# Kernel tuning notes

Hardware: AMD Instinct MI355X
Metric: run time of the kernel (lower is better)

Reference implementation:

```python
import jax, jax.numpy as jnp
import numpy as np

B, T = 16, 512
LAT, ACT, TSK = 512, 64, 96
E, NH, HD = 1024, 16, 64
L, HID, MAXS = 4, 4096, 512


def setup_inputs() -> dict:
    key = jax.random.key(0)
    ks = jax.random.split(key, 16)
    def rn(k, shape, std=0.02):
        return jax.random.normal(k, shape, jnp.float32) * std
    return {
        "z": jax.random.normal(ks[0], (B, T, LAT), jnp.float32),
        "a": jax.random.normal(ks[1], (B, T, ACT), jnp.float32),
        "task_emb": jax.random.normal(ks[2], (B, T, TSK), jnp.float32),
        "input_proj_w": rn(ks[3], (LAT + ACT + TSK, E)),
        "input_proj_b": jnp.zeros((E,), jnp.float32),
        "pos_emb": rn(ks[4], (1, MAXS, E)),
        "ln1_w": jnp.ones((L, E), jnp.float32),
        "ln1_b": jnp.zeros((L, E), jnp.float32),
        "qkv_w": rn(ks[5], (L, E, 3 * E)),
        "proj_w": rn(ks[6], (L, E, E)),
        "proj_b": jnp.zeros((L, E), jnp.float32),
        "ln2_w": jnp.ones((L, E), jnp.float32),
        "ln2_b": jnp.zeros((L, E), jnp.float32),
        "mlp_w1": rn(ks[7], (L, E, HID)),
        "mlp_b1": jnp.zeros((L, HID), jnp.float32),
        "mlp_w2": rn(ks[8], (L, HID, E)),
        "mlp_b2": jnp.zeros((L, E), jnp.float32),
        "out_norm_w": jnp.ones((E,), jnp.float32),
        "out_norm_b": jnp.zeros((E,), jnp.float32),
        "delta_w": rn(ks[9], (E, LAT)),
        "delta_b": jnp.zeros((LAT,), jnp.float32),
    }


def _ln(x, w, b, eps=1e-5):
    mu = jnp.mean(x, -1, keepdims=True)
    var = jnp.mean((x - mu) ** 2, -1, keepdims=True)
    return (x - mu) * jax.lax.rsqrt(var + eps) * w + b


def reference(z, a, task_emb, input_proj_w, input_proj_b, pos_emb,
              ln1_w, ln1_b, qkv_w, proj_w, proj_b, ln2_w, ln2_b,
              mlp_w1, mlp_b1, mlp_w2, mlp_b2,
              out_norm_w, out_norm_b, delta_w, delta_b):
    Bv, Tv, _ = z.shape
    x = jnp.concatenate([z, a, task_emb], axis=-1) @ input_proj_w + input_proj_b
    x = x + pos_emb[:, :Tv]
    scale = HD ** -0.5
    causal = jnp.tril(jnp.ones((Tv, Tv), bool))  # seq_start=0, no cache
    for l in range(L):
        h = _ln(x, ln1_w[l], ln1_b[l])
        qkv = (h @ qkv_w[l]).reshape(Bv, Tv, 3, NH, HD)
        q = jnp.swapaxes(qkv[:, :, 0], 1, 2) * scale  # (B,H,T,D)
        k = jnp.swapaxes(qkv[:, :, 1], 1, 2)
        v = jnp.swapaxes(qkv[:, :, 2], 1, 2)
        attn = jnp.einsum('bhqd,bhkd->bhqk', q, k)
        attn = jnp.where(causal, attn, -jnp.inf)
        attn = jax.nn.softmax(attn, axis=-1)
        o = jnp.einsum('bhqk,bhkd->bhqd', attn, v)
        o = jnp.swapaxes(o, 1, 2).reshape(Bv, Tv, E)
        x = x + (o @ proj_w[l] + proj_b[l])
        h2 = _ln(x, ln2_w[l], ln2_b[l])
        mid = jax.nn.gelu(h2 @ mlp_w1[l] + mlp_b1[l], approximate=False)
        x = x + (mid @ mlp_w2[l] + mlp_b2[l])
    x = _ln(x, out_norm_w, out_norm_b)
    return z + (x @ delta_w + delta_b)
```

## Files before the change

kernel.cpp:

```cpp
#include <hip/hip_runtime.h>
#include <hip/hip_bf16.h>
#include <math.h>

typedef unsigned short u16;
typedef unsigned int u32;
typedef __attribute__((ext_vector_type(4))) float f32x4;
typedef __attribute__((ext_vector_type(8))) short bf16x8;

#define DEV static __device__ __forceinline__

DEV u16 f2bf(float f) {
  __hip_bfloat16 h = __float2bfloat16(f);
  union { __hip_bfloat16 h; u16 u; } c; c.h = h; return c.u;
}

DEV void gload16(const void* g, void* l) {
  __builtin_amdgcn_global_load_lds((const __attribute__((address_space(1))) u32*)g,
                                   (__attribute__((address_space(3))) u32*)l, 16, 0, 0);
}

__global__ void transpose_w(const float* __restrict__ src, u16* __restrict__ dst,
                            int R, int C, int Rp) {
  __shared__ float tile[32][33];
  int tx = threadIdx.x, ty = threadIdx.y;
  int c0 = blockIdx.x * 32, r0 = blockIdx.y * 32;
  #pragma unroll
  for (int j = 0; j < 4; j++) {
    int r = r0 + ty + j * 8, c = c0 + tx;
    tile[ty + j * 8][tx] = (r < R && c < C) ? src[(size_t)r * C + c] : 0.f;
  }
  __syncthreads();
  #pragma unroll
  for (int j = 0; j < 4; j++) {
    int cc = c0 + ty + j * 8;
    int rr = r0 + tx;
    if (cc < C && rr < Rp) dst[(size_t)cc * Rp + rr] = f2bf(tile[tx][ty + j * 8]);
  }
}

__global__ void concat_k(const float* __restrict__ z, const float* __restrict__ a,
                         const float* __restrict__ te, u16* __restrict__ A) {
  const int total = 8192 * 704;
  for (int idx = blockIdx.x * 256 + threadIdx.x; idx < total; idx += gridDim.x * 256) {
    int m = idx / 704;
    int j = idx - m * 704;
    float v = 0.f;
    if (j < 512) v = z[(size_t)m * 512 + j];
    else if (j < 576) v = a[(size_t)m * 64 + (j - 512)];
    else if (j < 672) v = te[(size_t)m * 96 + (j - 576)];
    A[idx] = f2bf(v);
  }
}

__global__ __launch_bounds__(256) void ln_k(const float* __restrict__ x,
                                            const float* __restrict__ w,
                                            const float* __restrict__ b,
                                            u16* __restrict__ h) {
  int row = blockIdx.x * 4 + (threadIdx.x >> 6);
  int lane = threadIdx.x & 63;
  const float4* xr = (const float4*)(x + (size_t)row * 1024);
  float4 v[4]; float s = 0.f, sq = 0.f;
  #pragma unroll
  for (int i = 0; i < 4; i++) {
    v[i] = xr[lane + i * 64];
    s += v[i].x + v[i].y + v[i].z + v[i].w;
    sq += v[i].x * v[i].x + v[i].y * v[i].y + v[i].z * v[i].z + v[i].w * v[i].w;
  }
  #pragma unroll
  for (int off = 32; off >= 1; off >>= 1) { s += __shfl_xor(s, off); sq += __shfl_xor(sq, off); }
  float mean = s * (1.f / 1024.f);
  float var = sq * (1.f / 1024.f) - mean * mean;
  float rstd = rsqrtf(var + 1e-5f);
  const float4* wv = (const float4*)w;
  const float4* bv = (const float4*)b;
  u32* hr = (u32*)(h + (size_t)row * 1024);
  #pragma unroll
  for (int i = 0; i < 4; i++) {
    int idx = lane + i * 64;
    float4 wi = wv[idx], bi = bv[idx];
    float o0 = (v[i].x - mean) * rstd * wi.x + bi.x;
    float o1 = (v[i].y - mean) * rstd * wi.y + bi.y;
    float o2 = (v[i].z - mean) * rstd * wi.z + bi.z;
    float o3 = (v[i].w - mean) * rstd * wi.w + bi.w;
    hr[idx * 2]     = (u32)f2bf(o0) | ((u32)f2bf(o1) << 16);
    hr[idx * 2 + 1] = (u32)f2bf(o2) | ((u32)f2bf(o3) << 16);
  }
}

template <int FM, int EPI>
__global__ __launch_bounds__(512, 2) void gemm8(
    const u16* __restrict__ A, const u16* __restrict__ BT,
    float* __restrict__ outF, u16* __restrict__ outH,
    const float* __restrict__ bias, const float* __restrict__ res,
    const float* __restrict__ pos, int M, int N, int K, int gx) {
  constexpr int BM = FM * 32;
  constexpr int ABYTES = BM * 64;
  constexpr int BBYTES = 256 * 64;
  constexpr int SLICE = ABYTES + BBYTES;
  constexpr int LA = ABYTES / 8192;
  constexpr int LB = 2;
  __shared__ char lds[4 * SLICE];

  const int tid = threadIdx.x, lane = tid & 63, w = tid >> 6;
  const int wr = w >> 2, wc = w & 3;

  const int nwg = gridDim.x, orig = blockIdx.x;
  const int q = nwg >> 3, r = nwg & 7;
  const int xcd = orig & 7, loc = orig >> 3;
  const int sid = (xcd < r ? xcd * (q + 1) : r * (q + 1) + (xcd - r) * q) + loc;
  const int m0 = (sid / gx) * BM, n0 = (sid % gx) * 256;

  const char* Ag = (const char*)(A + (size_t)m0 * K);
  const char* Bg = (const char*)(BT + (size_t)n0 * K);
  const int Krow = K * 2;

  int aoff[LA], boff[LB];
  #pragma unroll
  for (int l = 0; l < LA; l++) {
    int c = l * 512 + tid, rw = c >> 2, g = (c & 3) ^ ((rw >> 1) & 3);
    aoff[l] = rw * Krow + g * 16;
  }
  #pragma unroll
  for (int l = 0; l < LB; l++) {
    int c = l * 512 + tid, rw = c >> 2, g = (c & 3) ^ ((rw >> 1) & 3);
    boff[l] = rw * Krow + g * 16;
  }
  const int ra = wr * (FM * 16) + (lane & 15);
  const int aRd = ra * 64 + (((lane >> 4) ^ ((ra >> 1) & 3)) << 4);
  const int rb = wc * 64 + (lane & 15);
  const int bRd = rb * 64 + (((lane >> 4) ^ ((rb >> 1) & 3)) << 4);

  f32x4 zero4 = {0.f, 0.f, 0.f, 0.f};
  f32x4 acc[FM][4];
  #pragma unroll
  for (int m = 0; m < FM; m++)
    #pragma unroll
    for (int n = 0; n < 4; n++) acc[m][n] = zero4;

  auto stageA = [&](int s) {
    char* Ad = lds + (s & 3) * SLICE;
    const char* src = Ag + (size_t)s * 64;
    #pragma unroll
    for (int l = 0; l < LA; l++)
      gload16(src + aoff[l], Ad + (l * 512 + w * 64) * 16);
  };
  auto stageB = [&](int s) {
    char* Bd = lds + (s & 3) * SLICE + ABYTES;
    const char* src = Bg + (size_t)s * 64;
    #pragma unroll
    for (int l = 0; l < LB; l++)
      gload16(src + boff[l], Bd + (l * 512 + w * 64) * 16);
  };

  const int NS = K >> 5;
  stageA(0); stageB(0); stageA(1); stageB(1);
  asm volatile("s_waitcnt vmcnt(3)" ::: "memory");
  __builtin_amdgcn_s_barrier();

  #pragma unroll 1
  for (int s = 0; s < NS; s++) {
    char* Ar = lds + (s & 3) * SLICE;
    char* Br = Ar + ABYTES;
    const bool pre = (s + 2 < NS);
    bf16x8 bfr[4], af[4];
    #pragma unroll
    for (int n = 0; n < 4; n++) bfr[n] = *(const bf16x8*)(Br + bRd + n * 1024);
    #pragma unroll
    for (int m = 0; m < 4; m++) af[m] = *(const bf16x8*)(Ar + aRd + m * 1024);
    if (pre) { stageA(s + 2); stageB(s + 2); }
    __builtin_amdgcn_sched_barrier(0);
    __builtin_amdgcn_s_barrier();
    asm volatile("s_waitcnt lgkmcnt(0)" ::: "memory");
    __builtin_amdgcn_sched_barrier(0);
    __builtin_amdgcn_s_setprio(1);
    #pragma unroll
    for (int m = 0; m < 4; m++)
      #pragma unroll
      for (int n = 0; n < 4; n++)
        acc[m][n] = __builtin_amdgcn_mfma_f32_16x16x32_bf16(af[m], bfr[n], acc[m][n], 0, 0, 0);
    __builtin_amdgcn_s_setprio(0);
    __builtin_amdgcn_sched_barrier(0);
    if (pre) asm volatile("s_waitcnt vmcnt(3)" ::: "memory");
    else     asm volatile("s_waitcnt vmcnt(0)" ::: "memory");
    __builtin_amdgcn_s_barrier();
  }

  #pragma unroll
  for (int m = 0; m < FM; m++) {
    #pragma unroll
    for (int i = 0; i < 4; i++) {
      int gm = m0 + wr * (FM * 16) + m * 16 + ((lane >> 4) << 2) + i;
      #pragma unroll
      for (int n = 0; n < 4; n++) {
        int gn = n0 + wc * 64 + n * 16 + (lane & 15);
        float v = acc[m][n][i];
        if (EPI & 1) v += bias[gn];
        if (EPI & 2) v += pos[(size_t)(gm & 511) * N + gn];
        if (EPI & 4) v += res[(size_t)gm * N + gn];
        if (EPI & 8) v = 0.5f * v * (1.f + erff(v * 0.70710678118654752f));
        if (EPI & 16) outH[(size_t)gm * N + gn] = f2bf(v);
        else outF[(size_t)gm * N + gn] = v;
      }
    }
  }
}

#define SB0 __builtin_amdgcn_sched_barrier(0)
#define VMW(N) asm volatile("s_waitcnt vmcnt(" #N ")" ::: "memory")
#define PH_TAIL(MFMAS) \
  SB0; __builtin_amdgcn_s_barrier(); \
  asm volatile("s_waitcnt lgkmcnt(0)" ::: "memory"); SB0; \
  __builtin_amdgcn_s_setprio(1); MFMAS; __builtin_amdgcn_s_setprio(0); \
  SB0; __builtin_amdgcn_s_barrier();
#define PH_TAILV(MFMAS, NN) \
  SB0; __builtin_amdgcn_s_barrier(); \
  asm volatile("s_waitcnt lgkmcnt(0)" ::: "memory"); SB0; \
  __builtin_amdgcn_s_setprio(1); MFMAS; __builtin_amdgcn_s_setprio(0); \
  SB0; VMW(NN); __builtin_amdgcn_s_barrier();
#define MM16(MB, BF) \
  _Pragma("unroll") \
  for (int mm = 0; mm < 4; mm++) \
    _Pragma("unroll") \
    for (int nn = 0; nn < 4; nn++) \
      acc[(MB) + mm][nn] = __builtin_amdgcn_mfma_f32_16x16x32_bf16(afr[mm], BF[nn], acc[(MB) + mm][nn], 0, 0, 0);
#define RD_A(BUF, K2L, MB) { \
  const char* _b = aRdB[BUF]; \
  afr[0] = *(const bf16x8*)(_b + aby[(MB) + 0][K2L]); \
  afr[1] = *(const bf16x8*)(_b + aby[(MB) + 1][K2L]); \
  afr[2] = *(const bf16x8*)(_b + aby[(MB) + 2][K2L]); \
  afr[3] = *(const bf16x8*)(_b + aby[(MB) + 3][K2L]); }
#define RD_BALL(BUF) { \
  const char* _b = bRdB[BUF]; \
  bfr0[0] = *(const bf16x8*)(_b + bby[0][0]); bfr1[0] = *(const bf16x8*)(_b + bby[0][1]); \
  bfr0[1] = *(const bf16x8*)(_b + bby[1][0]); bfr1[1] = *(const bf16x8*)(_b + bby[1][1]); \
  bfr0[2] = *(const bf16x8*)(_b + bby[2][0]); bfr1[2] = *(const bf16x8*)(_b + bby[2][1]); \
  bfr0[3] = *(const bf16x8*)(_b + bby[3][0]); bfr1[3] = *(const bf16x8*)(_b + bby[3][1]); }

template <int FM, int EPI>
__global__ __launch_bounds__(512, 2) void gemmP(
    const u16* __restrict__ A, const u16* __restrict__ BT,
    float* __restrict__ outF, u16* __restrict__ outH,
    const float* __restrict__ bias, const float* __restrict__ res,
    const float* __restrict__ pos, int M, int N, int K, int gx) {
  constexpr int RB = 16384;
  constexpr int NAREG = (FM == 8 ? 4 : 2);
  constexpr int BOFF = NAREG * RB;
  __shared__ char lds[BOFF + 4 * RB];

  const int tid = threadIdx.x, lane = tid & 63, w = tid >> 6;
  const int wr = w >> 2, wc = w & 3;
  const int ln = lane & 15, g = lane >> 4;

  const int nwg = gridDim.x, orig = blockIdx.x;
  const int q = nwg >> 3, r = nwg & 7;
  const int xcd = orig & 7, loc = orig >> 3;
  const int sid = (xcd < r ? xcd * (q + 1) : r * (q + 1) + (xcd - r) * q) + loc;
  const int m0 = (sid / gx) * (FM * 32), n0 = (sid % gx) * 256;

  const char* Ag = (const char*)(A + (size_t)m0 * K);
  const char* Bg = (const char*)(BT + (size_t)n0 * K);
  const size_t K2 = (size_t)K * 2;
  const int NT = K >> 6, NTm1 = NT - 1, NI = NT >> 1;

  int aby[FM][2], bby[4][2];
  #pragma unroll
  for (int m = 0; m < FM; m++) {
    int rr = (FM == 8 ? 0 : wr * 64) + m * 16 + ln;
    #pragma unroll
    for (int k2 = 0; k2 < 2; k2++)
      aby[m][k2] = rr * 128 + (((k2 * 4 + g) ^ (rr & 7)) << 4);
  }
  #pragma unroll
  for (int n = 0; n < 4; n++) {
    int rr = (wc & 1) * 64 + n * 16 + ln;
    #pragma unroll
    for (int k2 = 0; k2 < 2; k2++)
      bby[n][k2] = rr * 128 + (((k2 * 4 + g) ^ (rr & 7)) << 4);
  }
  const char* aRdB[2];
  const char* bRdB[2];
  if constexpr (FM == 8) {
    aRdB[0] = lds + (0 * 2 + wr) * RB;
    aRdB[1] = lds + (1 * 2 + wr) * RB;
  } else {
    aRdB[0] = lds;
    aRdB[1] = lds + RB;
  }
  bRdB[0] = lds + BOFF + (0 * 2 + (wc >> 1)) * RB;
  bRdB[1] = lds + BOFF + (1 * 2 + (wc >> 1)) * RB;

  int soff[2], sdst[2];
  #pragma unroll
  for (int l = 0; l < 2; l++) {
    int c = l * 512 + tid, rw = c >> 3, sl = c & 7;
    soff[l] = rw * (int)K2 + ((sl ^ (rw & 7)) << 4);
    sdst[l] = (l * 512 + w * 64) * 16;
  }

  auto stA = [&](int buf, int tau, int h) {
    char* d = lds + (FM == 8 ? (buf * 2 + h) : buf) * RB;
    const char* s = Ag + (size_t)(tau < NT ? tau : NTm1) * 128 + (FM == 8 ? (size_t)h * 128 * K2 : 0);
    #pragma unroll
    for (int l = 0; l < 2; l++) gload16(s + soff[l], d + sdst[l]);
  };
  auto stB = [&](int buf, int tau, int gg) {
    char* d = lds + BOFF + (buf * 2 + gg) * RB;
    const char* s = Bg + (size_t)(tau < NT ? tau : NTm1) * 128 + (size_t)gg * 128 * K2;
    #pragma unroll
    for (int l = 0; l < 2; l++) gload16(s + soff[l], d + sdst[l]);
  };

  f32x4 zero4 = {0.f, 0.f, 0.f, 0.f};
  f32x4 acc[FM][4];
  #pragma unroll
  for (int m = 0; m < FM; m++)
    #pragma unroll
    for (int n = 0; n < 4; n++) acc[m][n] = zero4;

  bf16x8 afr[4], bfr0[4], bfr1[4];

  if constexpr (FM == 8) {
    stA(0, 0, 0); stA(0, 0, 1); stB(0, 0, 0); stB(0, 0, 1); stB(1, 1, 0); stB(1, 1, 1);
    VMW(4);
    __builtin_amdgcn_s_barrier();
    #pragma unroll 1
    for (int J = 0; J < NI; J++) {
      const int t = 2 * J;
      RD_BALL(0); RD_A(0, 0, 0); stA(1, t + 1, 0);
      PH_TAIL(MM16(0, bfr0));
      RD_A(0, 0, 4); stA(1, t + 1, 1); stB(0, t + 2, 0);
      PH_TAIL(MM16(4, bfr0));
      RD_A(0, 1, 0); stB(0, t + 2, 1);
      PH_TAIL(MM16(0, bfr1));
      RD_A(0, 1, 4);
      PH_TAILV(MM16(4, bfr1), 4);
      RD_BALL(1); RD_A(1, 0, 0); stA(0, t + 2, 0);
      PH_TAIL(MM16(0, bfr0));
      RD_A(1, 0, 4); stA(0, t + 2, 1);
      PH_TAIL(MM16(4, bfr0));
      RD_A(1, 1, 0); stB(1, t + 3, 0);
      PH_TAIL(MM16(0, bfr1));
      RD_A(1, 1, 4); stB(1, t + 3, 1);
      PH_TAILV(MM16(4, bfr1), 4);
    }
  } else {
    stA(0, 0, 0); stB(0, 0, 0); stB(0, 0, 1); stB(1, 1, 0); stB(1, 1, 1);
    VMW(4);
    __builtin_amdgcn_s_barrier();
    #pragma unroll 1
    for (int J = 0; J < NI; J++) {
      const int t = 2 * J;
      RD_BALL(0); RD_A(0, 0, 0); stA(1, t + 1, 0);
      PH_TAIL(MM16(0, bfr0));
      RD_A(0, 1, 0); stB(0, t + 2, 0);
      PH_TAILV(MM16(0, bfr1), 2);
      RD_BALL(1); RD_A(1, 0, 0); stB(0, t + 2, 1); stA(0, t + 2, 0);
      PH_TAIL(MM16(0, bfr0));
      RD_A(1, 1, 0); stB(1, t + 3, 0); stB(1, t + 3, 1);
      PH_TAILV(MM16(0, bfr1), 4);
    }
  }
  VMW(0);

  #pragma unroll
  for (int m = 0; m < FM; m++) {
    #pragma unroll
    for (int i = 0; i < 4; i++) {
      int gm = m0 + wr * (FM * 16) + m * 16 + (g << 2) + i;
      #pragma unroll
      for (int n = 0; n < 4; n++) {
        int gn = n0 + wc * 64 + n * 16 + ln;
        float v = acc[m][n][i];
        if (EPI & 1) v += bias[gn];
        if (EPI & 2) v += pos[(size_t)(gm & 511) * N + gn];
        if (EPI & 4) v += res[(size_t)gm * N + gn];
        if (EPI & 8) v = 0.5f * v * (1.f + erff(v * 0.70710678118654752f));
        if (EPI & 16) outH[(size_t)gm * N + gn] = f2bf(v);
        else outF[(size_t)gm * N + gn] = v;
      }
    }
  }
}
#undef RD_BALL
#undef RD_A
#undef MM16
#undef PH_TAILV
#undef PH_TAIL
#undef VMW
#undef SB0

__global__ __launch_bounds__(512) void attn_k(const u16* __restrict__ qkv,
                                              u16* __restrict__ o) {
  __shared__ u16 Ks[512 * 64];
  __shared__ u16 Vt[64 * 512];
  __shared__ u16 Ps[8 * 512];
  const int tid = threadIdx.x, lane = tid & 63, w = tid >> 6;
  const int b = blockIdx.x >> 4, h = blockIdx.x & 15;
  const u16* base = qkv + (size_t)b * 512 * 3072 + h * 64;

  #pragma unroll
  for (int it = 0; it < 8; it++) {
    int chunk = it * 512 + tid;
    int row = chunk >> 3;
    int ib = (chunk & 7) * 16;
    int lb = ib ^ ((row & 7) << 4);
    gload16((const char*)(base + 1024 + (size_t)row * 3072) + lb,
            (char*)Ks + (it * 512 + w * 64) * 16);
  }
  {
    const u16* vrow = base + 2048 + (size_t)tid * 3072;
    #pragma unroll
    for (int c = 0; c < 8; c++) {
      uint4 u = *(const uint4*)(vrow + c * 8);
      u32 vals[4] = {u.x, u.y, u.z, u.w};
      #pragma unroll
      for (int pcompo = 0; pcompo < 4; pcompo++) {
        int d0 = c * 8 + pcompo * 2;
        size_t by0 = ((size_t)d0 * 1024 + tid * 2) ^ (size_t)((d0 & 7) << 4);
        size_t by1 = ((size_t)(d0 + 1) * 1024 + tid * 2) ^ (size_t)(((d0 + 1) & 7) << 4);
        *(u16*)((char*)Vt + by0) = (u16)(vals[pcompo] & 0xffff);
        *(u16*)((char*)Vt + by1) = (u16)(vals[pcompo] >> 16);
      }
    }
  }
  __syncthreads();

  const int qts[4] = {w, 15 - w, 16 + w, 31 - w};
  #pragma unroll
  for (int qi = 0; qi < 4; qi++) {
    const int qt = qts[qi];
    const int q0 = qt * 16;
    const int qcol = q0 + (lane & 15);
    const u16* qrow = base + (size_t)(q0 + (lane & 15)) * 3072 + ((lane >> 4) << 3);
    bf16x8 qf0 = *(const bf16x8*)qrow;
    bf16x8 qf1 = *(const bf16x8*)(qrow + 32);
    f32x4 zero4 = {0.f, 0.f, 0.f, 0.f};
    f32x4 oA[4] = {zero4, zero4, zero4, zero4};
    float mrun = -INFINITY, lrun = 0.f;
    const int nch = (qt >> 1) + 1;
    for (int ch = 0; ch < nch; ch++) {
      const int kb = ch * 32;
      f32x4 st0 = zero4, st1 = zero4;
      {
        int krow = kb + (lane & 15);
        int byc = krow * 128 + ((lane >> 4) << 4);
        int sw = (krow & 7) << 4;
        bf16x8 ka = *(const bf16x8*)((const char*)Ks + (byc ^ sw));
        bf16x8 kb2 = *(const bf16x8*)((const char*)Ks + ((byc + 64) ^ sw));
        st0 = __builtin_amdgcn_mfma_f32_16x16x32_bf16(ka, qf0, st0, 0, 0, 0);
        st0 = __builtin_amdgcn_mfma_f32_16x16x32_bf16(kb2, qf1, st0, 0, 0, 0);
      }
      {
        int krow = kb + 16 + (lane & 15);
        int byc = krow * 128 + ((lane >> 4) << 4);
        int sw = (krow & 7) << 4;
        bf16x8 ka = *(const bf16x8*)((const char*)Ks + (byc ^ sw));
        bf16x8 kb2 = *(const bf16x8*)((const char*)Ks + ((byc + 64) ^ sw));
        st1 = __builtin_amdgcn_mfma_f32_16x16x32_bf16(ka, qf0, st1, 0, 0, 0);
        st1 = __builtin_amdgcn_mfma_f32_16x16x32_bf16(kb2, qf1, st1, 0, 0, 0);
      }
      float sv[8]; float cmax = -INFINITY;
      #pragma unroll
      for (int i = 0; i < 4; i++) {
        int key0 = kb + ((lane >> 4) << 2) + i;
        float s0 = st0[i] * 0.125f; if (key0 > qcol) s0 = -INFINITY;
        float s1 = st1[i] * 0.125f; if (key0 + 16 > qcol) s1 = -INFINITY;
        sv[i] = s0; sv[4 + i] = s1;
        cmax = fmaxf(cmax, fmaxf(s0, s1));
      }
      cmax = fmaxf(cmax, __shfl_xor(cmax, 16));
      cmax = fmaxf(cmax, __shfl_xor(cmax, 32));
      float mnew = fmaxf(mrun, cmax);
      float corr = __expf(mrun - mnew);
      float pp[8]; float psum = 0.f;
      #pragma unroll
      for (int i = 0; i < 8; i++) { pp[i] = __expf(sv[i] - mnew); psum += pp[i]; }
      psum += __shfl_xor(psum, 16);
      psum += __shfl_xor(psum, 32);
      lrun = lrun * corr + psum;
      mrun = mnew;
      {
        int rowq = lane & 15;
        int pbase = w * 1024 + rowq * 64;
        int sw = (rowq & 3) << 4;
        uint2 t0, t1;
        t0.x = (u32)f2bf(pp[0]) | ((u32)f2bf(pp[1]) << 16);
        t0.y = (u32)f2bf(pp[2]) | ((u32)f2bf(pp[3]) << 16);
        t1.x = (u32)f2bf(pp[4]) | ((u32)f2bf(pp[5]) << 16);
        t1.y = (u32)f2bf(pp[6]) | ((u32)f2bf(pp[7]) << 16);
        int off0 = (((lane >> 4) << 3)) ^ sw;
        int off1 = (32 + ((lane >> 4) << 3)) ^ sw;
        *(uint2*)((char*)Ps + pbase + off0) = t0;
        *(uint2*)((char*)Ps + pbase + off1) = t1;
      }
      #pragma unroll
      for (int i = 0; i < 4; i++) {
        float fi = __shfl(corr, ((lane >> 4) << 2) + i);
        oA[0][i] *= fi; oA[1][i] *= fi; oA[2][i] *= fi; oA[3][i] *= fi;
      }
      {
        int rowq = lane & 15;
        int pby = w * 1024 + rowq * 64 + ((((lane >> 4) << 4)) ^ ((rowq & 3) << 4));
        bf16x8 pf = *(const bf16x8*)((const char*)Ps + pby);
        #pragma unroll
        for (int n = 0; n < 4; n++) {
          int d = n * 16 + (lane & 15);
          int vby = (d * 1024 + (kb + ((lane >> 4) << 3)) * 2) ^ ((d & 7) << 4);
          bf16x8 vf = *(const bf16x8*)((const char*)Vt + vby);
          oA[n] = __builtin_amdgcn_mfma_f32_16x16x32_bf16(pf, vf, oA[n], 0, 0, 0);
        }
      }
    }
    float inv = 1.f / lrun;
    #pragma unroll
    for (int i = 0; i < 4; i++) {
      float fi = __shfl(inv, ((lane >> 4) << 2) + i);
      int qr = q0 + ((lane >> 4) << 2) + i;
      size_t orow = ((size_t)b * 512 + qr) * 1024 + h * 64;
      #pragma unroll
      for (int n = 0; n < 4; n++)
        o[orow + n * 16 + (lane & 15)] = f2bf(oA[n][i] * fi);
    }
  }
}

extern "C" void kernel_launch(void* const* d_in, const int* in_sizes, int n_in,
                              void* d_out, int out_size, void* d_ws, size_t ws_size,
                              hipStream_t stream) {
  const float* z    = (const float*)d_in[0];
  const float* a    = (const float*)d_in[1];
  const float* te   = (const float*)d_in[2];
  const float* ipw  = (const float*)d_in[3];
  const float* ipb  = (const float*)d_in[4];
  const float* pos  = (const float*)d_in[5];
  const float* ln1w = (const float*)d_in[6];
  const float* ln1b = (const float*)d_in[7];
  const float* qkvw = (const float*)d_in[8];
  const float* projw= (const float*)d_in[9];
  const float* projb= (const float*)d_in[10];
  const float* ln2w = (const float*)d_in[11];
  const float* ln2b = (const float*)d_in[12];
  const float* w1   = (const float*)d_in[13];
  const float* b1   = (const float*)d_in[14];
  const float* w2   = (const float*)d_in[15];
  const float* b2   = (const float*)d_in[16];
  const float* onw  = (const float*)d_in[17];
  const float* onb  = (const float*)d_in[18];
  const float* dw   = (const float*)d_in[19];
  const float* db   = (const float*)d_in[20];
  float* out = (float*)d_out;

  char* p = (char*)d_ws;
  auto alloc = [&](size_t bytes) -> char* {
    char* r = p; p += (bytes + 255) & ~(size_t)255; return r;
  };
  u16* wt_in   = (u16*)alloc((size_t)1024 * 704 * 2);
  u16* wt_qkv  = (u16*)alloc((size_t)4 * 3072 * 1024 * 2);
  u16* wt_proj = (u16*)alloc((size_t)4 * 1024 * 1024 * 2);
  u16* wt_m1   = (u16*)alloc((size_t)4 * 4096 * 1024 * 2);
  u16* wt_m2   = (u16*)alloc((size_t)4 * 1024 * 4096 * 2);
  u16* wt_d    = (u16*)alloc((size_t)512 * 1024 * 2);
  u16* abuf    = (u16*)alloc((size_t)8192 * 704 * 2);
  float* xbuf  = (float*)alloc((size_t)8192 * 1024 * 4);
  u16* hbuf    = (u16*)alloc((size_t)8192 * 1024 * 2);
  u16* big     = (u16*)alloc((size_t)8192 * 4096 * 2);
  u16* obuf    = (u16*)alloc((size_t)8192 * 1024 * 2);
  u16* qkvb = big;
  u16* mid  = big;

  dim3 tb(32, 8);
  auto TR = [&](const float* s, u16* d, int R, int C, int Rp) {
    dim3 g((C + 31) / 32, (Rp + 31) / 32);
    transpose_w<<<g, tb, 0, stream>>>(s, d, R, C, Rp);
  };
  TR(ipw, wt_in, 672, 1024, 704);
  for (int l = 0; l < 4; l++) TR(qkvw + (size_t)l * 1024 * 3072, wt_qkv + (size_t)l * 3072 * 1024, 1024, 3072, 1024);
  for (int l = 0; l < 4; l++) TR(projw + (size_t)l * 1024 * 1024, wt_proj + (size_t)l * 1024 * 1024, 1024, 1024, 1024);
  for (int l = 0; l < 4; l++) TR(w1 + (size_t)l * 1024 * 4096, wt_m1 + (size_t)l * 4096 * 1024, 1024, 4096, 1024);
  for (int l = 0; l < 4; l++) TR(w2 + (size_t)l * 4096 * 1024, wt_m2 + (size_t)l * 1024 * 4096, 4096, 1024, 4096);
  TR(dw, wt_d, 1024, 512, 1024);

  concat_k<<<4096, 256, 0, stream>>>(z, a, te, abuf);

  gemm8<4, 3><<<4 * 64, 512, 0, stream>>>(abuf, wt_in, xbuf, nullptr, ipb, nullptr, pos, 8192, 1024, 704, 4);

  for (int l = 0; l < 4; l++) {
    ln_k<<<2048, 256, 0, stream>>>(xbuf, ln1w + l * 1024, ln1b + l * 1024, hbuf);
    gemmP<8, 16><<<384, 512, 0, stream>>>(hbuf, wt_qkv + (size_t)l * 3072 * 1024, nullptr, qkvb, nullptr, nullptr, nullptr, 8192, 3072, 1024, 12);
    attn_k<<<256, 512, 0, stream>>>(qkvb, obuf);
    gemmP<4, 5><<<256, 512, 0, stream>>>(obuf, wt_proj + (size_t)l * 1024 * 1024, xbuf, nullptr, projb + l * 1024, xbuf, nullptr, 8192, 1024, 1024, 4);
    ln_k<<<2048, 256, 0, stream>>>(xbuf, ln2w + l * 1024, ln2b + l * 1024, hbuf);
    gemmP<8, 25><<<512, 512, 0, stream>>>(hbuf, wt_m1 + (size_t)l * 4096 * 1024, nullptr, mid, b1 + l * 4096, nullptr, nullptr, 8192, 4096, 1024, 16);
    gemmP<4, 5><<<256, 512, 0, stream>>>(mid, wt_m2 + (size_t)l * 1024 * 4096, xbuf, nullptr, b2 + l * 1024, xbuf, nullptr, 8192, 1024, 4096, 4);
  }
  ln_k<<<2048, 256, 0, stream>>>(xbuf, onw, onb, hbuf);
  gemmP<4, 5><<<128, 512, 0, stream>>>(hbuf, wt_d, out, nullptr, db, z, nullptr, 8192, 512, 1024, 2);
}
```

Measured before the change: 1.452 ms.

## Use tanh-form GELU approximation and merge FM=8 GEMM phases into fewer barriers

Two changes. The exact erf-based GELU in the GEMM epilogues is replaced by a sigmoid/tanh-style approximation built on exp and a hardware reciprocal, which removes the costly erff call. In the FM=8 GEMM main loop, the eight half-K phases per iteration are merged into four. Each phase now reads both K halves of A and issues 32 MFMAs, which halves the number of barriers and waitcnt points but holds twice as many A fragments in registers. The approximation deviates from exact GELU, and the extra register pressure may hurt occupancy under launch_bounds(512,2).

```diff
diff --git a/kernel.cpp b/kernel.cpp
--- a/kernel.cpp
+++ b/kernel.cpp
@@ -12,6 +12,11 @@
 DEV u16 f2bf(float f) {
   __hip_bfloat16 h = __float2bfloat16(f);
   union { __hip_bfloat16 h; u16 u; } c; c.h = h; return c.u;
+}
+
+DEV float fast_gelu(float v) {
+  float u = v * (1.5957691216f + 0.0713548162f * v * v);
+  return v * __builtin_amdgcn_rcpf(1.f + __expf(-u));
 }
 
 DEV void gload16(const void* g, void* l) {
@@ -197,7 +202,7 @@
         if (EPI & 1) v += bias[gn];
         if (EPI & 2) v += pos[(size_t)(gm & 511) * N + gn];
         if (EPI & 4) v += res[(size_t)gm * N + gn];
-        if (EPI & 8) v = 0.5f * v * (1.f + erff(v * 0.70710678118654752f));
+        if (EPI & 8) v = fast_gelu(v);
         if (EPI & 16) outH[(size_t)gm * N + gn] = f2bf(v);
         else outF[(size_t)gm * N + gn] = v;
       }
@@ -222,13 +227,32 @@
   for (int mm = 0; mm < 4; mm++) \
     _Pragma("unroll") \
     for (int nn = 0; nn < 4; nn++) \
-      acc[(MB) + mm][nn] = __builtin_amdgcn_mfma_f32_16x16x32_bf16(afr[mm], BF[nn], acc[(MB) + mm][nn], 0, 0, 0);
-#define RD_A(BUF, K2L, MB) { \
+      acc[(MB) + mm][nn] = __builtin_amdgcn_mfma_f32_16x16x32_bf16(afr[mm][0], BF[nn], acc[(MB) + mm][nn], 0, 0, 0);
+#define MM32(MB) \
+  _Pragma("unroll") \
+  for (int kk2 = 0; kk2 < 2; kk2++) \
+    _Pragma("unroll") \
+    for (int mm = 0; mm < 4; mm++) \
+      _Pragma("unroll") \
+      for (int nn = 0; nn < 4; nn++) \
+        acc[(MB) + mm][nn] = __builtin_amdgcn_mfma_f32_16x16x32_bf16( \
+            afr[mm][kk2], kk2 ? bfr1[nn] : bfr0[nn], acc[(MB) + mm][nn], 0, 0, 0);
+#define RD_A1(BUF, K2L, MB) { \
   const char* _b = aRdB[BUF]; \
-  afr[0] = *(const bf16x8*)(_b + aby[(MB) + 0][K2L]); \
-  afr[1] = *(const bf16x8*)(_b + aby[(MB) + 1][K2L]); \
-  afr[2] = *(const bf16x8*)(_b + aby[(MB) + 2][K2L]); \
-  afr[3] = *(const bf16x8*)(_b + aby[(MB) + 3][K2L]); }
+  afr[0][0] = *(const bf16x8*)(_b + aby[(MB) + 0][K2L]); \
+  afr[1][0] = *(const bf16x8*)(_b + aby[(MB) + 1][K2L]); \
+  afr[2][0] = *(const bf16x8*)(_b + aby[(MB) + 2][K2L]); \
+  afr[3][0] = *(const bf16x8*)(_b + aby[(MB) + 3][K2L]); }
+#define RD_A8(BUF, MB) { \
+  const char* _b = aRdB[BUF]; \
+  afr[0][0] = *(const bf16x8*)(_b + aby[(MB) + 0][0]); \
+  afr[0][1] = *(const bf16x8*)(_b + aby[(MB) + 0][1]); \
+  afr[1][0] = *(const bf16x8*)(_b + aby[(MB) + 1][0]); \
+  afr[1][1] = *(const bf16x8*)(_b + aby[(MB) + 1][1]); \
+  afr[2][0] = *(const bf16x8*)(_b + aby[(MB) + 2][0]); \
+  afr[2][1] = *(const bf16x8*)(_b + aby[(MB) + 2][1]); \
+  afr[3][0] = *(const bf16x8*)(_b + aby[(MB) + 3][0]); \
+  afr[3][1] = *(const bf16x8*)(_b + aby[(MB) + 3][1]); }
 #define RD_BALL(BUF) { \
   const char* _b = bRdB[BUF]; \
   bfr0[0] = *(const bf16x8*)(_b + bby[0][0]); bfr1[0] = *(const bf16x8*)(_b + bby[0][1]); \
@@ -317,7 +341,7 @@
     #pragma unroll
     for (int n = 0; n < 4; n++) acc[m][n] = zero4;
 
-  bf16x8 afr[4], bfr0[4], bfr1[4];
+  bf16x8 afr[4][2], bfr0[4], bfr1[4];
 
   if constexpr (FM == 8) {
     stA(0, 0, 0); stA(0, 0, 1); stB(0, 0, 0); stB(0, 0, 1); stB(1, 1, 0); stB(1, 1, 1);
@@ -326,22 +350,14 @@
     #pragma unroll 1
     for (int J = 0; J < NI; J++) {
       const int t = 2 * J;
-      RD_BALL(0); RD_A(0, 0, 0); stA(1, t + 1, 0);
-      PH_TAIL(MM16(0, bfr0));
-      RD_A(0, 0, 4); stA(1, t + 1, 1); stB(0, t + 2, 0);
-      PH_TAIL(MM16(4, bfr0));
-      RD_A(0, 1, 0); stB(0, t + 2, 1);
-      PH_TAIL(MM16(0, bfr1));
-      RD_A(0, 1, 4);
-      PH_TAILV(MM16(4, bfr1), 4);
-      RD_BALL(1); RD_A(1, 0, 0); stA(0, t + 2, 0);
-      PH_TAIL(MM16(0, bfr0));
-      RD_A(1, 0, 4); stA(0, t + 2, 1);
-      PH_TAIL(MM16(4, bfr0));
-      RD_A(1, 1, 0); stB(1, t + 3, 0);
-      PH_TAIL(MM16(0, bfr1));
-      RD_A(1, 1, 4); stB(1, t + 3, 1);
-      PH_TAILV(MM16(4, bfr1), 4);
+      RD_BALL(0); RD_A8(0, 0); stA(1, t + 1, 0); stA(1, t + 1, 1);
+      PH_TAIL(MM32(0));
+      RD_A8(0, 4); stB(0, t + 2, 0); stB(0, t + 2, 1);
+      PH_TAILV(MM32(4), 4);
+      RD_BALL(1); RD_A8(1, 0); stA(0, t + 2, 0); stA(0, t + 2, 1);
+      PH_TAIL(MM32(0));
+      RD_A8(1, 4); stB(1, t + 3, 0); stB(1, t + 3, 1);
+      PH_TAILV(MM32(4), 4);
     }
   } else {
     stA(0, 0, 0); stB(0, 0, 0); stB(0, 0, 1); stB(1, 1, 0); stB(1, 1, 1);
@@ -350,13 +366,13 @@
     #pragma unroll 1
     for (int J = 0; J < NI; J++) {
       const int t = 2 * J;
-      RD_BALL(0); RD_A(0, 0, 0); stA(1, t + 1, 0);
+      RD_BALL(0); RD_A1(0, 0, 0); stA(1, t + 1, 0);
       PH_TAIL(MM16(0, bfr0));
-      RD_A(0, 1, 0); stB(0, t + 2, 0);
+      RD_A1(0, 1, 0); stB(0, t + 2, 0);
       PH_TAILV(MM16(0, bfr1), 2);
-      RD_BALL(1); RD_A(1, 0, 0); stB(0, t + 2, 1); stA(0, t + 2, 0);
+      RD_BALL(1); RD_A1(1, 0, 0); stB(0, t + 2, 1); stA(0, t + 2, 0);
       PH_TAIL(MM16(0, bfr0));
-      RD_A(1, 1, 0); stB(1, t + 3, 0); stB(1, t + 3, 1);
+      RD_A1(1, 1, 0); stB(1, t + 3, 0); stB(1, t + 3, 1);
       PH_TAILV(MM16(0, bfr1), 4);
     }
   }
@@ -374,7 +390,7 @@
         if (EPI & 1) v += bias[gn];
         if (EPI & 2) v += pos[(size_t)(gm & 511) * N + gn];
         if (EPI & 4) v += res[(size_t)gm * N + gn];
-        if (EPI & 8) v = 0.5f * v * (1.f + erff(v * 0.70710678118654752f));
+        if (EPI & 8) v = fast_gelu(v);
         if (EPI & 16) outH[(size_t)gm * N + gn] = f2bf(v);
         else outF[(size_t)gm * N + gn] = v;
       }
@@ -382,7 +398,9 @@
   }
 }
 #undef RD_BALL
-#undef RD_A
+#undef RD_A8
+#undef RD_A1
+#undef MM32
 #undef MM16
 #undef PH_TAILV
 #undef PH_TAIL
```

New measurement: 1.372 ms. 1.06x faster.
